# Kernel optimization log

Hardware: AMD Instinct MI355X
Metric: run time of the kernel (lower is better)

Reference implementation:

```python
import jax, jax.numpy as jnp
import numpy as np

THRESH = 0.7
MIN_KEPT_FRAC = 0.5  # max(0.001, 0.5)
LOG_CLAMP = -100.0   # torch BCELoss clamps log terms at -100


def setup_inputs() -> dict:
    key = jax.random.key(0)
    k1, k2 = jax.random.split(key)
    shape = (32, 1, 1024, 1024)
    pred = jax.random.uniform(k1, shape, dtype=jnp.float32, minval=1e-6, maxval=1.0 - 1e-6)
    target = jnp.round(jax.random.uniform(k2, shape, dtype=jnp.float32))  # binary mask
    return {"pred": pred, "target": target}


def reference(pred, target):
    p = pred.reshape(-1)
    t = target.reshape(-1)
    # elementwise BCE with reduction='none' (torch clamps log at -100)
    log_p = jnp.clip(jnp.log(p), LOG_CLAMP, None)
    log_1mp = jnp.clip(jnp.log1p(-p), LOG_CLAMP, None)
    pixel_losses = -(t * log_p + (1.0 - t) * log_1mp)

    n = p.shape[0]
    min_kept = min(int(MIN_KEPT_FRAC * (n - 1)), n - 1)  # static python int
    p_sorted = jnp.sort(p)
    min_value = p_sorted[min_kept]
    threshold = jnp.maximum(min_value, jnp.float32(THRESH))

    # keeping losses whose pred value is below the threshold; mean over kept
    mask = p < threshold
    cnt = jnp.sum(mask).astype(pixel_losses.dtype)
    return jnp.sum(jnp.where(mask, pixel_losses, 0.0)) / cnt
```

## Files before the change

kernel.cpp:

```cpp
#include <hip/hip_runtime.h>

#define THRESH   0.7f
#define BASEU    0x3F333334u
#define NBINS    2048
#define NSUB     4096
#define NTHREADS 256
#define MAXBLK   8192
#define NBLK_FB  1024

typedef __attribute__((ext_vector_type(4))) float f32x4;

struct Blk { float sum_lt; unsigned cnt_lt, cnt_eq, pad; };

struct Ws {
  Blk      blk[MAXBLK];
  double   sum_lt, sum_eq, prefix_sum;
  unsigned cnt_lt, cnt_eq;
  unsigned done;
  unsigned fin0, fin1, fin2, fin3;
  unsigned selBin, rank_r, prefix_cnt;
  unsigned Hcnt[NBINS];
  float    Hsum[NBINS];
  unsigned subCnt[NSUB];
  float    subSum[NSUB];
};

__device__ __forceinline__ float bce_loss(float p, float t) {
  float x = (t > 0.5f) ? p : (1.0f - p);
  return fminf(-__logf(x), 100.0f);
}

__global__ void k_main(
    const f32x4* __restrict__ p4, const f32x4* __restrict__ t4,
    Ws* __restrict__ ws, int n) {
  const int nvec = n >> 2;
  const int tid = blockIdx.x * NTHREADS + threadIdx.x;
  const int stride = gridDim.x * NTHREADS;

  float s_lt = 0.f;
  unsigned c_lt = 0u, c_eq = 0u;

  for (int i = tid; i < nvec; i += stride) {
    f32x4 p = __builtin_nontemporal_load(p4 + i);
    f32x4 t = __builtin_nontemporal_load(t4 + i);
#pragma unroll
    for (int c = 0; c < 4; ++c) {
      float pv = p[c];
      float x  = (t[c] > 0.5f) ? pv : (1.0f - pv);
      float l  = fminf(-__logf(x), 100.0f);
      bool lt  = (pv <  THRESH);
      s_lt += lt ? l : 0.0f;
      c_lt += lt ? 1u : 0u;
      c_eq += (pv == THRESH) ? 1u : 0u;
    }
  }
  {
    int i = (nvec << 2) + tid;
    if (i < n) {
      float pv = ((const float*)p4)[i];
      float l = bce_loss(pv, ((const float*)t4)[i]);
      if (pv < THRESH) { c_lt++; s_lt += l; }
      else if (pv == THRESH) { c_eq++; }
    }
  }

#pragma unroll
  for (int off = 32; off > 0; off >>= 1) {
    s_lt += __shfl_down(s_lt, off);
    c_lt += __shfl_down(c_lt, off);
    c_eq += __shfl_down(c_eq, off);
  }
  __shared__ float    red_slt[4];
  __shared__ unsigned red_clt[4], red_ceq[4];
  int wave = threadIdx.x >> 6;
  if ((threadIdx.x & 63) == 0) {
    red_slt[wave] = s_lt; red_clt[wave] = c_lt; red_ceq[wave] = c_eq;
  }
  __syncthreads();
  if (threadIdx.x == 0) {
    Blk b;
    b.sum_lt = red_slt[0] + red_slt[1] + red_slt[2] + red_slt[3];
    b.cnt_lt = red_clt[0] + red_clt[1] + red_clt[2] + red_clt[3];
    b.cnt_eq = red_ceq[0] + red_ceq[1] + red_ceq[2] + red_ceq[3];
    b.pad = 0u;
    ws->blk[blockIdx.x] = b;
  }
}

__global__ __launch_bounds__(1024) void k_decide(
    float* __restrict__ out, Ws* __restrict__ ws, int nblk, int kidx) {
  double s_lt = 0.0;
  unsigned long long c_lt = 0, c_eq = 0;
  for (int i = threadIdx.x; i < nblk; i += 1024) {
    Blk b = ws->blk[i];
    s_lt += (double)b.sum_lt;
    c_lt += b.cnt_lt; c_eq += b.cnt_eq;
  }
#pragma unroll
  for (int off = 32; off > 0; off >>= 1) {
    s_lt += __shfl_down(s_lt, off);
    c_lt += __shfl_down(c_lt, off);
    c_eq += __shfl_down(c_eq, off);
  }
  __shared__ double rs[16];
  __shared__ unsigned long long rc[16], re[16];
  int wave = threadIdx.x >> 6;
  if ((threadIdx.x & 63) == 0) { rs[wave] = s_lt; rc[wave] = c_lt; re[wave] = c_eq; }
  __syncthreads();
  if (threadIdx.x == 0) {
    double slt = 0.0; unsigned long long clt = 0, ceq = 0;
    for (int w = 0; w < 16; ++w) { slt += rs[w]; clt += rc[w]; ceq += re[w]; }
    ws->sum_lt = slt; ws->sum_eq = 0.0;
    ws->cnt_lt = (unsigned)clt; ws->cnt_eq = (unsigned)ceq;
    ws->fin0 = 0u; ws->fin1 = 0u; ws->fin2 = 0u; ws->fin3 = 0u;
    if (clt + ceq > (unsigned long long)kidx) {
      out[0] = (float)(slt / (double)clt);
      ws->done = 1u;
    } else {
      ws->done = 0u;
    }
  }
}

__device__ void gsync(unsigned* ctr, unsigned goal) {
  __syncthreads();
  if (threadIdx.x == 0) {
    __threadfence();
    atomicAdd(ctr, 1u);
    while (atomicAdd(ctr, 0u) < goal) __builtin_amdgcn_s_sleep(8);
  }
  __syncthreads();
  __threadfence();
}

__global__ __launch_bounds__(NTHREADS) void k_fallback(
    const float* __restrict__ pred, const float* __restrict__ targ,
    float* __restrict__ out, Ws* __restrict__ ws, int n, int kidx) {
  if (ws->done) return;

  __shared__ union {
    struct { unsigned hc[NBINS]; float hs[NBINS]; } l1;
    struct { unsigned sc[NSUB];  float ss[NSUB];  } l2;
  } sh;
  __shared__ float sh_eq;

  const int gtid = blockIdx.x * NTHREADS + threadIdx.x;
  const int gstride = gridDim.x * NTHREADS;

  for (int i = gtid; i < NBINS; i += gstride) { ws->Hcnt[i] = 0u; ws->Hsum[i] = 0.f; }
  for (int i = gtid; i < NSUB;  i += gstride) { ws->subCnt[i] = 0u; ws->subSum[i] = 0.f; }
  gsync(&ws->fin0, gridDim.x);

  for (int i = threadIdx.x; i < NBINS; i += NTHREADS) { sh.l1.hc[i] = 0u; sh.l1.hs[i] = 0.f; }
  if (threadIdx.x == 0) sh_eq = 0.f;
  __syncthreads();
  for (int i = gtid; i < n; i += gstride) {
    float pv = pred[i];
    if (pv >= THRESH) {
      float l = bce_loss(pv, targ[i]);
      if (pv == THRESH) {
        atomicAdd(&sh_eq, l);
      } else {
        unsigned b = (__float_as_uint(pv) - BASEU) >> 12;
        if (b > NBINS - 1) b = NBINS - 1;
        atomicAdd(&sh.l1.hc[b], 1u);
        atomicAdd(&sh.l1.hs[b], l);
      }
    }
  }
  __syncthreads();
  for (int i = threadIdx.x; i < NBINS; i += NTHREADS) {
    if (sh.l1.hc[i])        atomicAdd(&ws->Hcnt[i], sh.l1.hc[i]);
    if (sh.l1.hs[i] != 0.f) atomicAdd(&ws->Hsum[i], sh.l1.hs[i]);
  }
  if (threadIdx.x == 0 && sh_eq != 0.f) atomicAdd(&ws->sum_eq, (double)sh_eq);
  gsync(&ws->fin1, gridDim.x);

  if (blockIdx.x == 0 && threadIdx.x == 0) {
    unsigned long long cum = (unsigned long long)ws->cnt_lt + ws->cnt_eq;
    double csum = ws->sum_lt + ws->sum_eq;
    for (int b = 0; b < NBINS; ++b) {
      unsigned hcnt = atomicAdd(&ws->Hcnt[b], 0u);
      if (cum + hcnt > (unsigned long long)kidx) {
        atomicExch(&ws->selBin, (unsigned)b);
        atomicExch(&ws->rank_r, (unsigned)((unsigned long long)kidx - cum));
        atomicExch(&ws->prefix_cnt, (unsigned)cum);
        ws->prefix_sum = csum;
        break;
      }
      cum  += hcnt;
      csum += (double)atomicAdd(&ws->Hsum[b], 0.f);
    }
  }
  gsync(&ws->fin2, gridDim.x);

  unsigned base = BASEU + (atomicAdd(&ws->selBin, 0u) << 12);
  for (int i = threadIdx.x; i < NSUB; i += NTHREADS) { sh.l2.sc[i] = 0u; sh.l2.ss[i] = 0.f; }
  __syncthreads();
  for (int i = gtid; i < n; i += gstride) {
    unsigned u = __float_as_uint(pred[i]);
    if (u >= base && u < base + NSUB) {
      atomicAdd(&sh.l2.sc[u - base], 1u);
      atomicAdd(&sh.l2.ss[u - base], bce_loss(pred[i], targ[i]));
    }
  }
  __syncthreads();
  for (int i = threadIdx.x; i < NSUB; i += NTHREADS) {
    if (sh.l2.sc[i])         atomicAdd(&ws->subCnt[i], sh.l2.sc[i]);
    if (sh.l2.ss[i] != 0.f)  atomicAdd(&ws->subSum[i], sh.l2.ss[i]);
  }
  gsync(&ws->fin3, gridDim.x);

  if (blockIdx.x == 0 && threadIdx.x == 0) {
    unsigned r = atomicAdd(&ws->rank_r, 0u);
    unsigned long long cum = 0;
    double csum = 0.0;
    for (int i = 0; i < NSUB; ++i) {
      unsigned c = atomicAdd(&ws->subCnt[i], 0u);
      if (cum + c > (unsigned long long)r) {
        unsigned long long cnt_final = (unsigned long long)atomicAdd(&ws->prefix_cnt, 0u) + cum;
        double sum_final = ws->prefix_sum + csum;
        out[0] = (float)(sum_final / (double)cnt_final);
        break;
      }
      cum  += c;
      csum += (double)atomicAdd(&ws->subSum[i], 0.f);
    }
  }
}

__global__ void k_probe1(const f32x4* __restrict__ p4, Ws* __restrict__ ws, int nvec) {
  const int tid = blockIdx.x * NTHREADS + threadIdx.x;
  const int stride = gridDim.x * NTHREADS;
  f32x4 acc = {0.f, 0.f, 0.f, 0.f};
  for (int i = tid; i < nvec; i += stride) acc += p4[i];
  float s = acc.x + acc.y + acc.z + acc.w;
#pragma unroll
  for (int off = 32; off > 0; off >>= 1) s += __shfl_down(s, off);
  if (threadIdx.x == 0) ws->subSum[blockIdx.x & (NSUB - 1)] = s;
}

__global__ void k_probe2(const f32x4* __restrict__ p4, const f32x4* __restrict__ t4,
                         Ws* __restrict__ ws, int nvec) {
  const int tid = blockIdx.x * NTHREADS + threadIdx.x;
  const int stride = gridDim.x * NTHREADS;
  f32x4 acc = {0.f, 0.f, 0.f, 0.f};
  for (int i = tid; i < nvec; i += stride) acc += p4[i] + t4[i];
  float s = acc.x + acc.y + acc.z + acc.w;
#pragma unroll
  for (int off = 32; off > 0; off >>= 1) s += __shfl_down(s, off);
  if (threadIdx.x == 0) ws->subCnt[blockIdx.x & (NSUB - 1)] = __float_as_uint(s);
}

extern "C" void kernel_launch(void* const* d_in, const int* in_sizes, int n_in,
                              void* d_out, int out_size, void* d_ws, size_t ws_size,
                              hipStream_t stream) {
  const float* pred = (const float*)d_in[0];
  const float* targ = (const float*)d_in[1];
  float* out = (float*)d_out;
  Ws* ws = (Ws*)d_ws;
  int n = in_sizes[0];
  long long kll = (long long)(n - 1) / 2;
  if (kll > (long long)(n - 1)) kll = n - 1;
  int kidx = (int)kll;

  int nvec = n >> 2;
  int nblk = (nvec + NTHREADS - 1) / NTHREADS;
  if (nblk > MAXBLK) nblk = MAXBLK;
  if (nblk < 1) nblk = 1;

  k_main    <<<nblk, NTHREADS, 0, stream>>>((const f32x4*)pred, (const f32x4*)targ, ws, n);
  k_decide  <<<1, 1024, 0, stream>>>(out, ws, nblk, kidx);
  k_fallback<<<NBLK_FB, NTHREADS, 0, stream>>>(pred, targ, out, ws, n, kidx);
  k_probe1  <<<nblk, NTHREADS, 0, stream>>>((const f32x4*)pred, ws, nvec);
  k_probe2  <<<nblk, NTHREADS, 0, stream>>>((const f32x4*)pred, (const f32x4*)targ, ws, nvec);
}
```

Before: 321.0 us.

## Drop probe kernels, unroll main loads eightfold, and use log2 with a deferred ln2 scale

Removes the two probe kernels, which re-read the full pred and target arrays after the main pass. Each thread of the main kernel now issues eight vector loads of each input up front, with an asm barrier that keeps the loads grouped, and the grid shrinks to match. The loss uses log2 and multiplies the total by ln2 once in the decide step instead of calling natural log per element. Dropping the nontemporal hints and grid-stride loop could change caching behaviour. Since the probe kernels were debug traffic, most of the gain comes from no longer reading the inputs three times.

New measurement: 279.7 us. 1.15x faster.

```diff
diff --git a/kernel.cpp b/kernel.cpp
--- a/kernel.cpp
+++ b/kernel.cpp
@@ -5,8 +5,11 @@
 #define NBINS    2048
 #define NSUB     4096
 #define NTHREADS 256
+#define UNR      8
 #define MAXBLK   8192
 #define NBLK_FB  1024
+#define LOG2CLAMP 144.2695040888963f
+#define LN2_HI   0.6931471805599453
 
 typedef __attribute__((ext_vector_type(4))) float f32x4;
 
@@ -34,35 +37,59 @@
     const f32x4* __restrict__ p4, const f32x4* __restrict__ t4,
     Ws* __restrict__ ws, int n) {
   const int nvec = n >> 2;
-  const int tid = blockIdx.x * NTHREADS + threadIdx.x;
-  const int stride = gridDim.x * NTHREADS;
+  const int i0 = blockIdx.x * (NTHREADS * UNR) + threadIdx.x;
 
   float s_lt = 0.f;
   unsigned c_lt = 0u, c_eq = 0u;
 
-  for (int i = tid; i < nvec; i += stride) {
-    f32x4 p = __builtin_nontemporal_load(p4 + i);
-    f32x4 t = __builtin_nontemporal_load(t4 + i);
+#define CONS(PV, TV)                                                           \
+  _Pragma("unroll") for (int c = 0; c < 4; ++c) {                              \
+    float pv = (PV)[c];                                                        \
+    float xx = ((TV)[c] > 0.5f) ? pv : (1.0f - pv);                            \
+    float l2 = fminf(-__log2f(xx), LOG2CLAMP);                                 \
+    bool lt  = (pv < THRESH);                                                  \
+    s_lt += lt ? l2 : 0.0f;                                                    \
+    c_lt += lt ? 1u : 0u;                                                      \
+    c_eq += (pv == THRESH) ? 1u : 0u;                                          \
+  }
+
+  if (i0 + (UNR - 1) * NTHREADS < nvec) {
+    f32x4 pv0 = p4[i0 + 0 * NTHREADS], pv1 = p4[i0 + 1 * NTHREADS],
+          pv2 = p4[i0 + 2 * NTHREADS], pv3 = p4[i0 + 3 * NTHREADS],
+          pv4 = p4[i0 + 4 * NTHREADS], pv5 = p4[i0 + 5 * NTHREADS],
+          pv6 = p4[i0 + 6 * NTHREADS], pv7 = p4[i0 + 7 * NTHREADS];
+    f32x4 tv0 = t4[i0 + 0 * NTHREADS], tv1 = t4[i0 + 1 * NTHREADS],
+          tv2 = t4[i0 + 2 * NTHREADS], tv3 = t4[i0 + 3 * NTHREADS],
+          tv4 = t4[i0 + 4 * NTHREADS], tv5 = t4[i0 + 5 * NTHREADS],
+          tv6 = t4[i0 + 6 * NTHREADS], tv7 = t4[i0 + 7 * NTHREADS];
+    asm volatile("" ::
+        "v"(pv0), "v"(pv1), "v"(pv2), "v"(pv3),
+        "v"(pv4), "v"(pv5), "v"(pv6), "v"(pv7),
+        "v"(tv0), "v"(tv1), "v"(tv2), "v"(tv3),
+        "v"(tv4), "v"(tv5), "v"(tv6), "v"(tv7));
+    CONS(pv0, tv0) CONS(pv1, tv1) CONS(pv2, tv2) CONS(pv3, tv3)
+    CONS(pv4, tv4) CONS(pv5, tv5) CONS(pv6, tv6) CONS(pv7, tv7)
+  } else {
 #pragma unroll
-    for (int c = 0; c < 4; ++c) {
-      float pv = p[c];
-      float x  = (t[c] > 0.5f) ? pv : (1.0f - pv);
-      float l  = fminf(-__logf(x), 100.0f);
-      bool lt  = (pv <  THRESH);
-      s_lt += lt ? l : 0.0f;
-      c_lt += lt ? 1u : 0u;
-      c_eq += (pv == THRESH) ? 1u : 0u;
-    }
-  }
-  {
-    int i = (nvec << 2) + tid;
-    if (i < n) {
+    for (int u = 0; u < UNR; ++u) {
+      int id = i0 + u * NTHREADS;
+      if (id < nvec) {
+        f32x4 p = p4[id];
+        f32x4 t = t4[id];
+        CONS(p, t)
+      }
+    }
+    int i = (nvec << 2) + threadIdx.x;
+    if (blockIdx.x == gridDim.x - 1 && i < n) {
       float pv = ((const float*)p4)[i];
-      float l = bce_loss(pv, ((const float*)t4)[i]);
-      if (pv < THRESH) { c_lt++; s_lt += l; }
+      float tv = ((const float*)t4)[i];
+      float xx = (tv > 0.5f) ? pv : (1.0f - pv);
+      float l2 = fminf(-__log2f(xx), LOG2CLAMP);
+      if (pv < THRESH)       { c_lt++; s_lt += l2; }
       else if (pv == THRESH) { c_eq++; }
     }
   }
+#undef CONS
 
 #pragma unroll
   for (int off = 32; off > 0; off >>= 1) {
@@ -110,6 +137,7 @@
   if (threadIdx.x == 0) {
     double slt = 0.0; unsigned long long clt = 0, ceq = 0;
     for (int w = 0; w < 16; ++w) { slt += rs[w]; clt += rc[w]; ceq += re[w]; }
+    slt *= LN2_HI;
     ws->sum_lt = slt; ws->sum_eq = 0.0;
     ws->cnt_lt = (unsigned)clt; ws->cnt_eq = (unsigned)ceq;
     ws->fin0 = 0u; ws->fin1 = 0u; ws->fin2 = 0u; ws->fin3 = 0u;
@@ -229,29 +257,6 @@
   }
 }
 
-__global__ void k_probe1(const f32x4* __restrict__ p4, Ws* __restrict__ ws, int nvec) {
-  const int tid = blockIdx.x * NTHREADS + threadIdx.x;
-  const int stride = gridDim.x * NTHREADS;
-  f32x4 acc = {0.f, 0.f, 0.f, 0.f};
-  for (int i = tid; i < nvec; i += stride) acc += p4[i];
-  float s = acc.x + acc.y + acc.z + acc.w;
-#pragma unroll
-  for (int off = 32; off > 0; off >>= 1) s += __shfl_down(s, off);
-  if (threadIdx.x == 0) ws->subSum[blockIdx.x & (NSUB - 1)] = s;
-}
-
-__global__ void k_probe2(const f32x4* __restrict__ p4, const f32x4* __restrict__ t4,
-                         Ws* __restrict__ ws, int nvec) {
-  const int tid = blockIdx.x * NTHREADS + threadIdx.x;
-  const int stride = gridDim.x * NTHREADS;
-  f32x4 acc = {0.f, 0.f, 0.f, 0.f};
-  for (int i = tid; i < nvec; i += stride) acc += p4[i] + t4[i];
-  float s = acc.x + acc.y + acc.z + acc.w;
-#pragma unroll
-  for (int off = 32; off > 0; off >>= 1) s += __shfl_down(s, off);
-  if (threadIdx.x == 0) ws->subCnt[blockIdx.x & (NSUB - 1)] = __float_as_uint(s);
-}
-
 extern "C" void kernel_launch(void* const* d_in, const int* in_sizes, int n_in,
                               void* d_out, int out_size, void* d_ws, size_t ws_size,
                               hipStream_t stream) {
@@ -265,13 +270,11 @@
   int kidx = (int)kll;
 
   int nvec = n >> 2;
-  int nblk = (nvec + NTHREADS - 1) / NTHREADS;
+  int nblk = (nvec + NTHREADS * UNR - 1) / (NTHREADS * UNR);
   if (nblk > MAXBLK) nblk = MAXBLK;
   if (nblk < 1) nblk = 1;
 
   k_main    <<<nblk, NTHREADS, 0, stream>>>((const f32x4*)pred, (const f32x4*)targ, ws, n);
   k_decide  <<<1, 1024, 0, stream>>>(out, ws, nblk, kidx);
   k_fallback<<<NBLK_FB, NTHREADS, 0, stream>>>(pred, targ, out, ws, n, kidx);
-  k_probe1  <<<nblk, NTHREADS, 0, stream>>>((const f32x4*)pred, ws, nvec);
-  k_probe2  <<<nblk, NTHREADS, 0, stream>>>((const f32x4*)pred, (const f32x4*)targ, ws, nvec);
-}
+}
```
